# Kernel tuning notes

Measured on AMD Instinct MI355X. Metric: run time of the kernel, lower is better.

Reference implementation:

```python
import jax, jax.numpy as jnp
import numpy as np

B, N, D_IN, D_OUT, R = 8, 2048, 256, 256, 4


def setup_inputs() -> dict:
    key = jax.random.key(0)
    k1, k2, k3, k4 = jax.random.split(key, 4)
    x = jax.random.normal(k1, (B, N, D_IN), dtype=jnp.float32)
    adj = jnp.zeros((1,), dtype=jnp.float32)  # unused by the module
    # relation-type matrix: 0 = no edge, 1..R = relation id
    relation = jax.random.randint(k2, (B, N, N), 0, R + 1, dtype=jnp.int32)
    weight = jax.random.normal(k3, (R, D_IN, D_OUT), dtype=jnp.float32) * 0.05
    bias = jax.random.normal(k4, (D_OUT,), dtype=jnp.float32) * 0.05
    return {"x": x, "adj": adj, "relation": relation, "weight": weight, "bias": bias}


def reference(x, adj, relation, weight, bias):
    # Binary per-relation adjacency masks: [R, B, N, N]
    rel_ids = jnp.arange(1, weight.shape[0] + 1, dtype=relation.dtype)
    masks = (relation[None] == rel_ids[:, None, None, None]).astype(x.dtype)
    # Aggregate neighbors per relation: h[r] = A_r @ x  -> [R, B, N, D_in]
    h = jnp.einsum('rbnm,bmd->rbnd', masks, x)
    # Per-relation output transform, summed over relations: [B, N, D_out]
    y = jnp.einsum('rbnd,rdo->bno', h, weight)
    return y + bias
```

## Files before the change

kernel.cpp:

```cpp
#include <hip/hip_runtime.h>
#include <hip/hip_bf16.h>
#include <stdint.h>

typedef uint32_t u32;
typedef uint64_t u64;
typedef __bf16 bf16x8 __attribute__((ext_vector_type(8)));
typedef float f32x4 __attribute__((ext_vector_type(4)));
typedef u32 u32x4 __attribute__((ext_vector_type(4)));

#define NB 8
#define NN 2048
#define DIN 256
#define DOUT 256
#define NR 4
#define KTOT (NN * NR)

#define XW_BYTES   (NB * DOUT * KTOT * 2)
#define PART_BYTES (NB * NN * DOUT * 4)
#define WT_BYTES   (NR * DIN * DOUT * 2)
#define PART_ELEMS (NB * NN * DOUT)

__device__ __forceinline__ ushort f2bf(float f) {
  union { float f; u32 u; } c; c.f = f;
  return (ushort)((c.u + 0x7FFFu + ((c.u >> 16) & 1u)) >> 16);
}

__device__ __forceinline__ float bf2f(ushort u) {
  union { u32 i; float f; } c; c.i = ((u32)u) << 16; return c.f;
}

__device__ __forceinline__ void gload_lds16(const void* g, void* l) {
  __builtin_amdgcn_global_load_lds(
      (const __attribute__((address_space(1))) u32*)g,
      (__attribute__((address_space(3))) u32*)l, 16, 0, 0);
}

__global__ void k0_wT(const float* __restrict__ w, ushort* __restrict__ wT) {
  int i = blockIdx.x * 256 + threadIdx.x;
  int o = i & 255, d = (i >> 8) & 255, r = i >> 16;
  wT[(r * DOUT + o) * DIN + d] = f2bf(w[i]);
}

__global__ __launch_bounds__(512) void k1_xw(const float* __restrict__ x,
                                             const ushort* __restrict__ wT,
                                             ushort* __restrict__ xwT) {
  __shared__ char smem[65536];
  ushort* As = (ushort*)smem;
  ushort* Bs = (ushort*)(smem + 4096);
  const int t = threadIdx.x, l = t & 63, w = t >> 6;
  const int r = w >> 1, oh = w & 1;
  const int blk = blockIdx.x;
  const int b = blk >> 6, rest = blk & 63, mc = rest >> 1, ot = rest & 1;

  f32x4 acc[4][4] = {};
  const int arow = t >> 3, adc = (t & 7) << 2;
  const float* xg = x + ((size_t)(b * NN + mc * 64 + arow) * DIN + adc);

  for (int s = 0; s < 8; ++s) {
    const int d0 = s * 32;
    float4 xv = *(const float4*)(xg + d0);
    ushort4 a4;
    a4.x = f2bf(xv.x); a4.y = f2bf(xv.y); a4.z = f2bf(xv.z); a4.w = f2bf(xv.w);
    *(ushort4*)(As + arow * 32 + adc) = a4;
#pragma unroll
    for (int i = 0; i < 4; ++i) {
      int off = i * 4096 + t * 8;
      int rr = off >> 12, rem = off & 4095, o = rem >> 5, dd = rem & 31;
      const ushort* src = wT + ((size_t)(rr * DOUT + ot * 128 + o) * DIN + d0 + dd);
      gload_lds16(src, Bs + off);
    }
    __syncthreads();
    bf16x8 af[4];
#pragma unroll
    for (int fm = 0; fm < 4; ++fm)
      af[fm] = *(const bf16x8*)(As + (fm * 16 + (l & 15)) * 32 + (l >> 4) * 8);
#pragma unroll
    for (int fo = 0; fo < 4; ++fo) {
      bf16x8 bf = *(const bf16x8*)(Bs + (size_t)(r * 128 + oh * 64 + fo * 16 + (l & 15)) * 32 + (l >> 4) * 8);
#pragma unroll
      for (int fm = 0; fm < 4; ++fm)
        acc[fm][fo] = __builtin_amdgcn_mfma_f32_16x16x32_bf16(af[fm], bf, acc[fm][fo], 0, 0, 0);
    }
    __syncthreads();
  }
  ushort* Cs = (ushort*)smem;
#pragma unroll
  for (int fm = 0; fm < 4; ++fm)
#pragma unroll
    for (int fo = 0; fo < 4; ++fo)
#pragma unroll
      for (int j = 0; j < 4; ++j) {
        int o_loc = oh * 64 + fo * 16 + (l & 15);
        int ml = fm * 16 + (l >> 4) * 4 + j;
        Cs[o_loc * 256 + ml * 4 + r] = f2bf(acc[fm][fo][j]);
      }
  __syncthreads();
#pragma unroll
  for (int i = 0; i < 8; ++i) {
    int el = (i * 512 + t) * 8;
    int o_loc = el >> 8, kp = el & 255;
    *(uint4*)(xwT + (size_t)(b * DOUT + ot * 128 + o_loc) * KTOT + mc * 256 + kp) =
        *(const uint4*)(Cs + el);
  }
}

__global__ __launch_bounds__(512, 2) void k2_v2(const int* __restrict__ rel,
                                                const ushort* __restrict__ xwT,
                                                ushort* __restrict__ partb) {
  __shared__ char smem[131072];
  const int t = threadIdx.x, l = t & 63, w = t >> 6;
  const int wm = w >> 2, wn = w & 3;
  const int logical = (blockIdx.x & 7) * 32 + (blockIdx.x >> 3);
  const int b = logical >> 5;
  const int nt = (logical >> 2) & 7;
  const int ks = logical & 3;

  f32x4 acc[8][4] = {};
  const int fr = l & 15, fq = l >> 4;
  const int rswz = (fr & 7) << 4;

  char* const Ab0 = smem;
  char* const Ab1 = smem + 32768;
  char* const Bb0 = smem + 65536;
  char* const Bb1 = smem + 98304;

  const int arow = t >> 1, half = t & 1;
  const int aswz = (arow & 7) << 4;
  const int* relg = rel + ((size_t)(b * NN + nt * 256 + arow)) * NN + ks * 512 + half * 8;

  const int brow = t >> 3;
  const int kd = (((t & 7) ^ ((t >> 3) & 7)) << 3);
  const ushort* xwb = xwT + (size_t)b * DOUT * KTOT + ks * 2048;

  int4 rs0a, rs0b, rs1a, rs1b;

#define GLD_ALL(S, BB)                                                         \
  {                                                                            \
    _Pragma("unroll") for (int i = 0; i < 4; ++i)                              \
      gload_lds16(xwb + (size_t)(brow + 64 * i) * KTOT + (S) * 64 + kd,        \
                  (BB) + i * 8192 + t * 16);                                   \
  }

#define RELLOAD(S, RA, RB)                                                     \
  RA = *(const int4*)(relg + (S) * 16);                                        \
  RB = *(const int4*)(relg + (S) * 16 + 4);

#define EXPAND_A(ABASE, V0, V1)                                                \
  {                                                                            \
    char* rowp = (ABASE) + arow * 128;                                         \
    int vv[8] = {V0.x, V0.y, V0.z, V0.w, V1.x, V1.y, V1.z, V1.w};              \
    _Pragma("unroll") for (int p = 0; p < 4; ++p) {                            \
      int va = vv[2 * p], vb = vv[2 * p + 1];                                  \
      u32 sa = ((u32)(va - 1) & 3u) * 16u;                                     \
      u32 sb = ((u32)(vb - 1) & 3u) * 16u;                                     \
      u64 ha = va ? (0x3F80ull << sa) : 0ull;                                  \
      u64 hb = vb ? (0x3F80ull << sb) : 0ull;                                  \
      u32x4 e = {(u32)ha, (u32)(ha >> 32), (u32)hb, (u32)(hb >> 32)};          \
      *(u32x4*)(rowp + ((half * 64 + p * 16) ^ aswz)) = e;                     \
    }                                                                          \
  }

#define RDB(BV, BB, KK)                                                        \
  _Pragma("unroll") for (int fo = 0; fo < 4; ++fo)                             \
    BV[fo] = *(const bf16x8*)((BB) + (wn * 64 + fo * 16 + fr) * 128 +          \
                              (((KK) * 64 + fq * 16) ^ rswz));

#define RDA(AV, AB, FM0, KK)                                                   \
  _Pragma("unroll") for (int i = 0; i < 4; ++i)                                \
    AV[i] = *(const bf16x8*)((AB) + (wm * 128 + ((FM0) + i) * 16 + fr) * 128 + \
                             (((KK) * 64 + fq * 16) ^ rswz));

#define MFMA4(FM0, AV, BV)                                                     \
  __builtin_amdgcn_s_setprio(1);                                               \
  _Pragma("unroll") for (int i = 0; i < 4; ++i)                                \
    _Pragma("unroll") for (int fo = 0; fo < 4; ++fo)                           \
      acc[(FM0) + i][fo] = __builtin_amdgcn_mfma_f32_16x16x32_bf16(            \
          AV[i], BV[fo], acc[(FM0) + i][fo], 0, 0, 0);                         \
  __builtin_amdgcn_s_setprio(0);

#define ENDFENCE(VMS)                                                          \
  asm volatile("s_waitcnt vmcnt(" VMS ") lgkmcnt(0)" ::: "memory");            \
  __builtin_amdgcn_s_barrier();                                                \
  __builtin_amdgcn_sched_barrier(0);

#define STEP(S, P, Q, STG, REL, EXP, VMS)                                      \
  {                                                                            \
    bf16x8 b0[4], b1[4], aA[4], aB[4], aC[4], aD[4];                           \
    RDB(b0, Bb##P, 0);                                                         \
    RDA(aA, Ab##P, 0, 0);                                                      \
    if (STG) { GLD_ALL((S) + 1, Bb##Q); }                                      \
    __builtin_amdgcn_sched_barrier(0);                                         \
    if (REL) { RELLOAD((S) + 2, rs##P##a, rs##P##b); }                         \
    RDA(aB, Ab##P, 4, 0);                                                      \
    MFMA4(0, aA, b0);                                                          \
    RDA(aC, Ab##P, 0, 1);                                                      \
    if (EXP) { EXPAND_A(Ab##Q, rs##Q##a, rs##Q##b); }                          \
    MFMA4(4, aB, b0);                                                          \
    RDB(b1, Bb##P, 1);                                                         \
    RDA(aD, Ab##P, 4, 1);                                                      \
    MFMA4(0, aC, b1);                                                          \
    MFMA4(4, aD, b1);                                                          \
    ENDFENCE(VMS);                                                             \
  }

  GLD_ALL(0, Bb0);
  __builtin_amdgcn_sched_barrier(0);
  RELLOAD(0, rs0a, rs0b);
  RELLOAD(1, rs1a, rs1b);
  EXPAND_A(Ab0, rs0a, rs0b);
  ENDFENCE("4");

  for (int s = 0; s < 30; s += 2) {
    STEP(s, 0, 1, 1, 1, 1, "2");
    STEP(s + 1, 1, 0, 1, 1, 1, "2");
  }
  STEP(30, 0, 1, 1, 0, 1, "0");
  {
    bf16x8 b0[4], b1[4], aA[4], aB[4], aC[4], aD[4];
    RDB(b0, Bb1, 0);
    RDA(aA, Ab1, 0, 0);
    RDA(aB, Ab1, 4, 0);
    MFMA4(0, aA, b0);
    RDA(aC, Ab1, 0, 1);
    MFMA4(4, aB, b0);
    RDB(b1, Bb1, 1);
    RDA(aD, Ab1, 4, 1);
    MFMA4(0, aC, b1);
    MFMA4(4, aD, b1);
  }

  ushort* dst = partb + (size_t)ks * PART_ELEMS;
#pragma unroll
  for (int fm = 0; fm < 8; ++fm)
#pragma unroll
    for (int fo = 0; fo < 4; ++fo) {
      int n = nt * 256 + wm * 128 + fm * 16 + fq * 4;
      int o = wn * 64 + fo * 16 + fr;
#pragma unroll
      for (int j = 0; j < 4; ++j)
        dst[(size_t)(b * NN + n + j) * DOUT + o] = f2bf(acc[fm][fo][j]);
    }
#undef STEP
#undef ENDFENCE
#undef MFMA4
#undef RDA
#undef RDB
#undef EXPAND_A
#undef RELLOAD
#undef GLD_ALL
}

__global__ void k3_sum(float* __restrict__ out, const ushort* __restrict__ partb,
                       const float* __restrict__ bias) {
  int i = blockIdx.x * 256 + threadIdx.x;
  float4 s = ((const float4*)bias)[i & 63];
#pragma unroll
  for (int p = 0; p < 4; ++p) {
    ushort4 v = ((const ushort4*)(partb + (size_t)p * PART_ELEMS))[i];
    s.x += bf2f(v.x); s.y += bf2f(v.y); s.z += bf2f(v.z); s.w += bf2f(v.w);
  }
  ((float4*)out)[i] = s;
}

__global__ __launch_bounds__(256, 2) void k2_r4(const int* __restrict__ rel,
                                                const ushort* __restrict__ xwT,
                                                float* __restrict__ out,
                                                float* __restrict__ part) {
  __shared__ char smem[81920];
  const int t = threadIdx.x, l = t & 63, w = t >> 6;
  const int wr = w >> 1, wc = w & 1;
  const int logical = (blockIdx.x & 7) * 64 + (blockIdx.x >> 3);
  const int b = logical >> 6;
  const int nt = (logical >> 2) & 15;
  const int ks = (logical >> 1) & 1;
  const int ot = logical & 1;

  f32x4 acc[4][4] = {};
  const int arow = t >> 1, half = t & 1;
  const int* relg = rel + ((size_t)(b * NN + nt * 128 + arow) * NN + ks * 1024 + half * 8);
  const ushort* xwb = xwT + (size_t)(b * DOUT + ot * 128) * KTOT + ks * 4096;

  char* const Ab0 = smem;
  char* const Ab1 = smem + 16384;
  char* const Bb0 = smem + 32768;
  char* const Bb1 = smem + 49152;
  char* const Bb2 = smem + 65536;

  const int brow = t >> 3;
  const int kd = (((t & 7) ^ ((t >> 3) & 7)) << 3);
  const int aswz = (arow & 7) << 4;
  const int fr = l & 15, fq = l >> 4;
  const int rswz = (fr & 7) << 4;

  int4 rsA0, rsB0, rsA1, rsB1;

#define STAGE_B(S, BBASE)                                                      \
  {                                                                            \
    _Pragma("unroll") for (int i = 0; i < 4; ++i)                              \
      gload_lds16(xwb + (size_t)(brow + 32 * i) * KTOT + (S) * 64 + kd,        \
                  (BBASE) + i * 4096 + t * 16);                                \
  }
#define RELLOAD(S, RA, RB)                                                     \
  RA = *(const int4*)(relg + (S) * 16);                                        \
  RB = *(const int4*)(relg + (S) * 16 + 4);
#define EXPAND_A(ABASE, V0, V1)                                                \
  {                                                                            \
    char* rowp = (ABASE) + arow * 128;                                         \
    int vv[8] = {V0.x, V0.y, V0.z, V0.w, V1.x, V1.y, V1.z, V1.w};              \
    _Pragma("unroll") for (int p = 0; p < 4; ++p) {                            \
      int va = vv[2 * p], vb = vv[2 * p + 1];                                  \
      u32 sa = ((u32)(va - 1) & 3u) * 16u;                                     \
      u32 sb = ((u32)(vb - 1) & 3u) * 16u;                                     \
      u64 ha = va ? (0x3F80ull << sa) : 0ull;                                  \
      u64 hb = vb ? (0x3F80ull << sb) : 0ull;                                  \
      u32x4 e = {(u32)ha, (u32)(ha >> 32), (u32)hb, (u32)(hb >> 32)};          \
      *(u32x4*)(rowp + ((half * 64 + p * 16) ^ aswz)) = e;                     \
    }                                                                          \
  }
#define BARV6()                                                                \
  asm volatile("s_waitcnt vmcnt(6) lgkmcnt(0)" ::: "memory");                  \
  __builtin_amdgcn_s_barrier();                                                \
  __builtin_amdgcn_sched_barrier(0);
#define BARV0()                                                                \
  asm volatile("s_waitcnt vmcnt(0) lgkmcnt(0)" ::: "memory");                  \
  __builtin_amdgcn_s_barrier();                                                \
  __builtin_amdgcn_sched_barrier(0);
#define MFMA_STEP(AC, BC)                                                      \
  __builtin_amdgcn_s_setprio(1);                                               \
  _Pragma("unroll") for (int kk = 0; kk < 2; ++kk) {                           \
    bf16x8 af[4], bfv[4];                                                      \
    const int colb = (kk * 64 + fq * 16) ^ rswz;                               \
    _Pragma("unroll") for (int fm = 0; fm < 4; ++fm)                           \
      af[fm] = *(const bf16x8*)((AC) + (wr * 64 + fm * 16 + fr) * 128 + colb); \
    _Pragma("unroll") for (int fo = 0; fo < 4; ++fo)                           \
      bfv[fo] = *(const bf16x8*)((BC) + (wc * 64 + fo * 16 + fr) * 128 + colb);\
    _Pragma("unroll") for (int fm = 0; fm < 4; ++fm)                           \
      _Pragma("unroll") for (int fo = 0; fo < 4; ++fo)                         \
        acc[fm][fo] = __builtin_amdgcn_mfma_f32_16x16x32_bf16(                 \
            af[fm], bfv[fo], acc[fm][fo], 0, 0, 0);                            \
  }                                                                            \
  __builtin_amdgcn_s_setprio(0);
#define BODY(S, ACUR, BCUR, ANXT, RLA, RLB, RCA, RCB, BSTG)                    \
  {                                                                            \
    STAGE_B((S) + 2, BSTG);                                                    \
    RELLOAD((S) + 2, RLA, RLB);                                                \
    MFMA_STEP(ACUR, BCUR);                                                     \
    EXPAND_A(ANXT, RCA, RCB);                                                  \
    BARV6();                                                                   \
  }

  STAGE_B(0, Bb0);
  RELLOAD(0, rsA0, rsB0);
  STAGE_B(1, Bb1);
  RELLOAD(1, rsA1, rsB1);
  EXPAND_A(Ab0, rsA0, rsB0);
  BARV6();

  for (int s = 0; s < 60; s += 6) {
    BODY(s + 0, Ab0, Bb0, Ab1, rsA0, rsB0, rsA1, rsB1, Bb2);
    BODY(s + 1, Ab1, Bb1, Ab0, rsA1, rsB1, rsA0, rsB0, Bb0);
    BODY(s + 2, Ab0, Bb2, Ab1, rsA0, rsB0, rsA1, rsB1, Bb1);
    BODY(s + 3, Ab1, Bb0, Ab0, rsA1, rsB1, rsA0, rsB0, Bb2);
    BODY(s + 4, Ab0, Bb1, Ab1, rsA0, rsB0, rsA1, rsB1, Bb0);
    BODY(s + 5, Ab1, Bb2, Ab0, rsA1, rsB1, rsA0, rsB0, Bb1);
  }
  BODY(60, Ab0, Bb0, Ab1, rsA0, rsB0, rsA1, rsB1, Bb2);
  BODY(61, Ab1, Bb1, Ab0, rsA1, rsB1, rsA0, rsB0, Bb0);
  {
    MFMA_STEP(Ab0, Bb2);
    EXPAND_A(Ab1, rsA1, rsB1);
    BARV0();
  }
  {
    MFMA_STEP(Ab1, Bb0);
  }

  float* dst = ks ? part : out;
#pragma unroll
  for (int fm = 0; fm < 4; ++fm)
#pragma unroll
    for (int fo = 0; fo < 4; ++fo) {
      int n = nt * 128 + wr * 64 + fm * 16 + fq * 4;
      int o = ot * 128 + wc * 64 + fo * 16 + fr;
#pragma unroll
      for (int j = 0; j < 4; ++j)
        dst[(size_t)(b * NN + n + j) * DOUT + o] = acc[fm][fo][j];
    }
#undef BODY
#undef MFMA_STEP
#undef BARV6
#undef BARV0
#undef EXPAND_A
#undef RELLOAD
#undef STAGE_B
}

__global__ void k3_r4(float* __restrict__ out, const float* __restrict__ part,
                      const float* __restrict__ bias) {
  int i = blockIdx.x * 256 + threadIdx.x;
  float4 o = ((const float4*)out)[i];
  float4 p = ((const float4*)part)[i];
  float4 bv = ((const float4*)bias)[i & 63];
  float4 rr;
  rr.x = o.x + p.x + bv.x;
  rr.y = o.y + p.y + bv.y;
  rr.z = o.z + p.z + bv.z;
  rr.w = o.w + p.w + bv.w;
  ((float4*)out)[i] = rr;
}

extern "C" void kernel_launch(void* const* d_in, const int* in_sizes, int n_in,
                              void* d_out, int out_size, void* d_ws, size_t ws_size,
                              hipStream_t stream) {
  const float* x = (const float*)d_in[0];
  const int* rel = (const int*)d_in[2];
  const float* wgt = (const float*)d_in[3];
  const float* bias = (const float*)d_in[4];
  float* out = (float*)d_out;
  char* ws = (char*)d_ws;

  const size_t partb_bytes = (size_t)PART_ELEMS * 2 * 4;
  const size_t need_big = (size_t)XW_BYTES + partb_bytes + WT_BYTES;
  if (ws_size >= need_big) {
    ushort* xwT = (ushort*)ws;
    ushort* partb = (ushort*)(ws + XW_BYTES);
    ushort* wT = (ushort*)(ws + XW_BYTES + partb_bytes);
    k0_wT<<<1024, 256, 0, stream>>>(wgt, wT);
    k1_xw<<<512, 512, 0, stream>>>(x, wT, xwT);
    k2_v2<<<256, 512, 0, stream>>>(rel, xwT, partb);
    k3_sum<<<4096, 256, 0, stream>>>(out, partb, bias);
  } else {
    ushort* xwT = (ushort*)ws;
    float* part = (float*)(ws + XW_BYTES);
    ushort* wT = (ushort*)(ws + XW_BYTES + PART_BYTES);
    k0_wT<<<1024, 256, 0, stream>>>(wgt, wT);
    k1_xw<<<512, 512, 0, stream>>>(x, wT, xwT);
    k2_r4<<<512, 256, 0, stream>>>(rel, xwT, out, part);
    k3_r4<<<4096, 256, 0, stream>>>(out, part, bias);
  }
}
```

Measured before the change: 110.3 us.

## Stream raw relation ints into LDS via async loads and expand one-hot in registers

The main GEMM kernel used to load relation ids into registers, expand them into bf16 one-hot rows and write those to LDS each step. It now copies raw int32 relation tiles straight into LDS with global_load_lds, reads them back as int2 pairs, and builds the one-hot bf16x8 A fragments in registers right before each MFMA. This removes the LDS write and expansion phase from the critical path and puts both operands on the async DMA path, with A buffers covering two k-steps. In exchange it adds per-MFMA ALU work to build fragments, a new pipeline schedule with different vmcnt fences, and a dropped lgkmcnt wait.

```diff
diff --git a/kernel.cpp b/kernel.cpp
--- a/kernel.cpp
+++ b/kernel.cpp
@@ -33,6 +33,16 @@
   __builtin_amdgcn_global_load_lds(
       (const __attribute__((address_space(1))) u32*)g,
       (__attribute__((address_space(3))) u32*)l, 16, 0, 0);
+}
+
+__device__ __forceinline__ bf16x8 onehot8(int v0, int v1) {
+  u32 sa = ((u32)(v0 - 1) & 3u) * 16u;
+  u32 sb = ((u32)(v1 - 1) & 3u) * 16u;
+  u64 ha = v0 ? (0x3F80ull << sa) : 0ull;
+  u64 hb = v1 ? (0x3F80ull << sb) : 0ull;
+  union { u32x4 u; bf16x8 b; } c;
+  c.u = (u32x4){(u32)ha, (u32)(ha >> 32), (u32)hb, (u32)(hb >> 32)};
+  return c.b;
 }
 
 __global__ void k0_wT(const float* __restrict__ w, ushort* __restrict__ wT) {
@@ -104,7 +114,7 @@
   }
 }
 
-__global__ __launch_bounds__(512, 2) void k2_v2(const int* __restrict__ rel,
+__global__ __launch_bounds__(512, 2) void k2_v3(const int* __restrict__ rel,
                                                 const ushort* __restrict__ xwT,
                                                 ushort* __restrict__ partb) {
   __shared__ char smem[131072];
@@ -124,40 +134,26 @@
   char* const Bb0 = smem + 65536;
   char* const Bb1 = smem + 98304;
 
-  const int arow = t >> 1, half = t & 1;
-  const int aswz = (arow & 7) << 4;
-  const int* relg = rel + ((size_t)(b * NN + nt * 256 + arow)) * NN + ks * 512 + half * 8;
+  const int arow4 = t >> 3;
+  const int acol = ((t & 7) ^ ((t >> 3) & 7)) * 4;
+  const int* relg0 = rel + ((size_t)(b * NN + nt * 256)) * NN + ks * 512;
 
   const int brow = t >> 3;
   const int kd = (((t & 7) ^ ((t >> 3) & 7)) << 3);
   const ushort* xwb = xwT + (size_t)b * DOUT * KTOT + ks * 2048;
 
-  int4 rs0a, rs0b, rs1a, rs1b;
-
-#define GLD_ALL(S, BB)                                                         \
+#define GLD_B(S, BB)                                                           \
   {                                                                            \
     _Pragma("unroll") for (int i = 0; i < 4; ++i)                              \
       gload_lds16(xwb + (size_t)(brow + 64 * i) * KTOT + (S) * 64 + kd,        \
                   (BB) + i * 8192 + t * 16);                                   \
   }
 
-#define RELLOAD(S, RA, RB)                                                     \
-  RA = *(const int4*)(relg + (S) * 16);                                        \
-  RB = *(const int4*)(relg + (S) * 16 + 4);
-
-#define EXPAND_A(ABASE, V0, V1)                                                \
-  {                                                                            \
-    char* rowp = (ABASE) + arow * 128;                                         \
-    int vv[8] = {V0.x, V0.y, V0.z, V0.w, V1.x, V1.y, V1.z, V1.w};              \
-    _Pragma("unroll") for (int p = 0; p < 4; ++p) {                            \
-      int va = vv[2 * p], vb = vv[2 * p + 1];                                  \
-      u32 sa = ((u32)(va - 1) & 3u) * 16u;                                     \
-      u32 sb = ((u32)(vb - 1) & 3u) * 16u;                                     \
-      u64 ha = va ? (0x3F80ull << sa) : 0ull;                                  \
-      u64 hb = vb ? (0x3F80ull << sb) : 0ull;                                  \
-      u32x4 e = {(u32)ha, (u32)(ha >> 32), (u32)hb, (u32)(hb >> 32)};          \
-      *(u32x4*)(rowp + ((half * 64 + p * 16) ^ aswz)) = e;                     \
-    }                                                                          \
+#define GLD_A(P, AB)                                                           \
+  {                                                                            \
+    _Pragma("unroll") for (int i = 0; i < 4; ++i)                              \
+      gload_lds16(relg0 + (size_t)(arow4 + 64 * i) * NN + (P) * 32 + acol,     \
+                  (AB) + i * 8192 + t * 16);                                   \
   }
 
 #define RDB(BV, BB, KK)                                                        \
@@ -165,68 +161,71 @@
     BV[fo] = *(const bf16x8*)((BB) + (wn * 64 + fo * 16 + fr) * 128 +          \
                               (((KK) * 64 + fq * 16) ^ rswz));
 
-#define RDA(AV, AB, FM0, KK)                                                   \
-  _Pragma("unroll") for (int i = 0; i < 4; ++i)                                \
-    AV[i] = *(const bf16x8*)((AB) + (wm * 128 + ((FM0) + i) * 16 + fr) * 128 + \
-                             (((KK) * 64 + fq * 16) ^ rswz));
-
-#define MFMA4(FM0, AV, BV)                                                     \
+#define RDAREL(AR, AB, SIG)                                                    \
+  _Pragma("unroll") for (int f = 0; f < 8; ++f)                                \
+    _Pragma("unroll") for (int kq = 0; kq < 2; ++kq)                           \
+      AR[f * 2 + kq] = *(const int2*)((AB) + (wm * 128 + f * 16 + fr) * 128 +  \
+                                      (((SIG) * 64 + kq * 32 + fq * 8) ^ rswz));
+
+#define MFMAQ(FM0, AR, BV, KK)                                                 \
   __builtin_amdgcn_s_setprio(1);                                               \
-  _Pragma("unroll") for (int i = 0; i < 4; ++i)                                \
+  _Pragma("unroll") for (int i = 0; i < 4; ++i) {                              \
+    bf16x8 af = onehot8(AR[((FM0) + i) * 2 + (KK)].x,                          \
+                        AR[((FM0) + i) * 2 + (KK)].y);                         \
     _Pragma("unroll") for (int fo = 0; fo < 4; ++fo)                           \
       acc[(FM0) + i][fo] = __builtin_amdgcn_mfma_f32_16x16x32_bf16(            \
-          AV[i], BV[fo], acc[(FM0) + i][fo], 0, 0, 0);                         \
+          af, BV[fo], acc[(FM0) + i][fo], 0, 0, 0);                            \
+  }                                                                            \
   __builtin_amdgcn_s_setprio(0);
 
-#define ENDFENCE(VMS)                                                          \
-  asm volatile("s_waitcnt vmcnt(" VMS ") lgkmcnt(0)" ::: "memory");            \
+#define ENDF(VMS)                                                              \
+  asm volatile("s_waitcnt vmcnt(" VMS ")" ::: "memory");                       \
   __builtin_amdgcn_s_barrier();                                                \
   __builtin_amdgcn_sched_barrier(0);
 
-#define STEP(S, P, Q, STG, REL, EXP, VMS)                                      \
-  {                                                                            \
-    bf16x8 b0[4], b1[4], aA[4], aB[4], aC[4], aD[4];                           \
-    RDB(b0, Bb##P, 0);                                                         \
-    RDA(aA, Ab##P, 0, 0);                                                      \
-    if (STG) { GLD_ALL((S) + 1, Bb##Q); }                                      \
+#define STEP(S, PAIR, SIG, AB, BB, BN, AN, STGB, STGA, VMS)                    \
+  {                                                                            \
+    bf16x8 bv0[4], bv1[4];                                                     \
+    int2 ar[16];                                                               \
+    RDB(bv0, BB, 0);                                                           \
+    RDAREL(ar, AB, SIG);                                                       \
+    if (STGB) { GLD_B((S) + 1, BN); }                                          \
+    if (STGA) { GLD_A((PAIR) + 1, AN); }                                       \
     __builtin_amdgcn_sched_barrier(0);                                         \
-    if (REL) { RELLOAD((S) + 2, rs##P##a, rs##P##b); }                         \
-    RDA(aB, Ab##P, 4, 0);                                                      \
-    MFMA4(0, aA, b0);                                                          \
-    RDA(aC, Ab##P, 0, 1);                                                      \
-    if (EXP) { EXPAND_A(Ab##Q, rs##Q##a, rs##Q##b); }                          \
-    MFMA4(4, aB, b0);                                                          \
-    RDB(b1, Bb##P, 1);                                                         \
-    RDA(aD, Ab##P, 4, 1);                                                      \
-    MFMA4(0, aC, b1);                                                          \
-    MFMA4(4, aD, b1);                                                          \
-    ENDFENCE(VMS);                                                             \
-  }
-
-  GLD_ALL(0, Bb0);
+    MFMAQ(0, ar, bv0, 0);                                                      \
+    MFMAQ(4, ar, bv0, 0);                                                      \
+    RDB(bv1, BB, 1);                                                           \
+    MFMAQ(0, ar, bv1, 1);                                                      \
+    MFMAQ(4, ar, bv1, 1);                                                      \
+    ENDF(VMS);                                                                 \
+  }
+
+  GLD_A(0, Ab0);
+  GLD_B(0, Bb0);
+  asm volatile("s_waitcnt vmcnt(0)" ::: "memory");
+  __builtin_amdgcn_s_barrier();
   __builtin_amdgcn_sched_barrier(0);
-  RELLOAD(0, rs0a, rs0b);
-  RELLOAD(1, rs1a, rs1b);
-  EXPAND_A(Ab0, rs0a, rs0b);
-  ENDFENCE("4");
-
-  for (int s = 0; s < 30; s += 2) {
-    STEP(s, 0, 1, 1, 1, 1, "2");
-    STEP(s + 1, 1, 0, 1, 1, 1, "2");
-  }
-  STEP(30, 0, 1, 1, 0, 1, "0");
+
+  for (int i = 0; i < 7; ++i) {
+    const int s = i * 4, p = i * 2;
+    STEP(s + 0, p + 0, 0, Ab0, Bb0, Bb1, Ab1, 1, 1, "4");
+    STEP(s + 1, p + 0, 1, Ab0, Bb1, Bb0, Ab0, 1, 0, "0");
+    STEP(s + 2, p + 1, 0, Ab1, Bb0, Bb1, Ab0, 1, 1, "4");
+    STEP(s + 3, p + 1, 1, Ab1, Bb1, Bb0, Ab0, 1, 0, "0");
+  }
+  STEP(28, 14, 0, Ab0, Bb0, Bb1, Ab1, 1, 1, "4");
+  STEP(29, 14, 1, Ab0, Bb1, Bb0, Ab0, 1, 0, "0");
+  STEP(30, 15, 0, Ab1, Bb0, Bb1, Ab0, 1, 0, "0");
   {
-    bf16x8 b0[4], b1[4], aA[4], aB[4], aC[4], aD[4];
-    RDB(b0, Bb1, 0);
-    RDA(aA, Ab1, 0, 0);
-    RDA(aB, Ab1, 4, 0);
-    MFMA4(0, aA, b0);
-    RDA(aC, Ab1, 0, 1);
-    MFMA4(4, aB, b0);
-    RDB(b1, Bb1, 1);
-    RDA(aD, Ab1, 4, 1);
-    MFMA4(0, aC, b1);
-    MFMA4(4, aD, b1);
+    bf16x8 bv0[4], bv1[4];
+    int2 ar[16];
+    RDB(bv0, Bb1, 0);
+    RDAREL(ar, Ab1, 1);
+    MFMAQ(0, ar, bv0, 0);
+    MFMAQ(4, ar, bv0, 0);
+    RDB(bv1, Bb1, 1);
+    MFMAQ(0, ar, bv1, 1);
+    MFMAQ(4, ar, bv1, 1);
   }
 
   ushort* dst = partb + (size_t)ks * PART_ELEMS;
@@ -241,13 +240,12 @@
         dst[(size_t)(b * NN + n + j) * DOUT + o] = f2bf(acc[fm][fo][j]);
     }
 #undef STEP
-#undef ENDFENCE
-#undef MFMA4
-#undef RDA
+#undef ENDF
+#undef MFMAQ
+#undef RDAREL
 #undef RDB
-#undef EXPAND_A
-#undef RELLOAD
-#undef GLD_ALL
+#undef GLD_A
+#undef GLD_B
 }
 
 __global__ void k3_sum(float* __restrict__ out, const ushort* __restrict__ partb,
@@ -427,7 +425,7 @@
     ushort* wT = (ushort*)(ws + XW_BYTES + partb_bytes);
     k0_wT<<<1024, 256, 0, stream>>>(wgt, wT);
     k1_xw<<<512, 512, 0, stream>>>(x, wT, xwT);
-    k2_v2<<<256, 512, 0, stream>>>(rel, xwT, partb);
+    k2_v3<<<256, 512, 0, stream>>>(rel, xwT, partb);
     k3_sum<<<4096, 256, 0, stream>>>(out, partb, bias);
   } else {
     ushort* xwT = (ushort*)ws;
```

New measurement: 123.2 us. +11.7%, slower.

## Store relation A-tile as byte masks in LDS and expand to bf16 in registers

Applied to the files above, without the earlier changes.

The k2 main kernel now keeps the one-hot relation A operand in shared memory as 8-bit masks instead of expanded bf16 values. This halves the A-tile LDS footprint (shared memory drops from 128KB to 96KB) and halves the A-side LDS read and write traffic. Each MFMA A fragment is rebuilt in registers with v_perm and an AND against the bf16 1.0 pattern. The cost is extra VALU work per MFMA, and the reads and MFMAs are now grouped into whole half-steps, which changes how LDS reads overlap with compute.

```diff
diff --git a/kernel.cpp b/kernel.cpp
--- a/kernel.cpp
+++ b/kernel.cpp
@@ -33,6 +33,10 @@
   __builtin_amdgcn_global_load_lds(
       (const __attribute__((address_space(1))) u32*)g,
       (__attribute__((address_space(3))) u32*)l, 16, 0, 0);
+}
+
+__device__ __forceinline__ u32 relmask(int v) {
+  return v ? (0xFFu << (((u32)(v - 1) & 3u) * 8u)) : 0u;
 }
 
 __global__ void k0_wT(const float* __restrict__ w, ushort* __restrict__ wT) {
@@ -104,10 +108,10 @@
   }
 }
 
-__global__ __launch_bounds__(512, 2) void k2_v2(const int* __restrict__ rel,
+__global__ __launch_bounds__(512, 2) void k2_v5(const int* __restrict__ rel,
                                                 const ushort* __restrict__ xwT,
                                                 ushort* __restrict__ partb) {
-  __shared__ char smem[131072];
+  __shared__ char smem[98304];
   const int t = threadIdx.x, l = t & 63, w = t >> 6;
   const int wm = w >> 2, wn = w & 3;
   const int logical = (blockIdx.x & 7) * 32 + (blockIdx.x >> 3);
@@ -120,13 +124,14 @@
   const int rswz = (fr & 7) << 4;
 
   char* const Ab0 = smem;
-  char* const Ab1 = smem + 32768;
-  char* const Bb0 = smem + 65536;
-  char* const Bb1 = smem + 98304;
+  char* const Ab1 = smem + 16384;
+  char* const Bb0 = smem + 32768;
+  char* const Bb1 = smem + 65536;
 
   const int arow = t >> 1, half = t & 1;
-  const int aswz = (arow & 7) << 4;
   const int* relg = rel + ((size_t)(b * NN + nt * 256 + arow)) * NN + ks * 512 + half * 8;
+  char* const rowA0 = Ab0 + arow * 64;
+  char* const rowA1 = Ab1 + arow * 64;
 
   const int brow = t >> 3;
   const int kd = (((t & 7) ^ ((t >> 3) & 7)) << 3);
@@ -145,18 +150,12 @@
   RA = *(const int4*)(relg + (S) * 16);                                        \
   RB = *(const int4*)(relg + (S) * 16 + 4);
 
-#define EXPAND_A(ABASE, V0, V1)                                                \
-  {                                                                            \
-    char* rowp = (ABASE) + arow * 128;                                         \
+#define EXPAND_M(ROWP, V0, V1)                                                 \
+  {                                                                            \
     int vv[8] = {V0.x, V0.y, V0.z, V0.w, V1.x, V1.y, V1.z, V1.w};              \
-    _Pragma("unroll") for (int p = 0; p < 4; ++p) {                            \
-      int va = vv[2 * p], vb = vv[2 * p + 1];                                  \
-      u32 sa = ((u32)(va - 1) & 3u) * 16u;                                     \
-      u32 sb = ((u32)(vb - 1) & 3u) * 16u;                                     \
-      u64 ha = va ? (0x3F80ull << sa) : 0ull;                                  \
-      u64 hb = vb ? (0x3F80ull << sb) : 0ull;                                  \
-      u32x4 e = {(u32)ha, (u32)(ha >> 32), (u32)hb, (u32)(hb >> 32)};          \
-      *(u32x4*)(rowp + ((half * 64 + p * 16) ^ aswz)) = e;                     \
+    _Pragma("unroll") for (int jj = 0; jj < 4; ++jj) {                         \
+      u64 mw = (u64)relmask(vv[2 * jj]) | ((u64)relmask(vv[2 * jj + 1]) << 32);\
+      *(u64*)((ROWP) + (((half * 4 + jj) ^ (arow & 7)) * 8)) = mw;             \
     }                                                                          \
   }
 
@@ -165,50 +164,58 @@
     BV[fo] = *(const bf16x8*)((BB) + (wn * 64 + fo * 16 + fr) * 128 +          \
                               (((KK) * 64 + fq * 16) ^ rswz));
 
-#define RDA(AV, AB, FM0, KK)                                                   \
-  _Pragma("unroll") for (int i = 0; i < 4; ++i)                                \
-    AV[i] = *(const bf16x8*)((AB) + (wm * 128 + ((FM0) + i) * 16 + fr) * 128 + \
-                             (((KK) * 64 + fq * 16) ^ rswz));
-
-#define MFMA4(FM0, AV, BV)                                                     \
+#define RDA_K(AR, AB, KK)                                                      \
+  _Pragma("unroll") for (int f = 0; f < 8; ++f)                                \
+    AR[f] = *(const int2*)((AB) + (wm * 128 + f * 16 + fr) * 64 +              \
+                           ((((KK) * 4 + fq) ^ (fr & 7)) * 8));
+
+#define MFMA1(FM, Q, BV)                                                       \
+  {                                                                            \
+    u32x4 uu;                                                                  \
+    uu.x = __builtin_amdgcn_perm((u32)(Q).x, (u32)(Q).x, 0x01010000u) & 0x3F803F80u; \
+    uu.y = __builtin_amdgcn_perm((u32)(Q).x, (u32)(Q).x, 0x03030202u) & 0x3F803F80u; \
+    uu.z = __builtin_amdgcn_perm((u32)(Q).y, (u32)(Q).y, 0x01010000u) & 0x3F803F80u; \
+    uu.w = __builtin_amdgcn_perm((u32)(Q).y, (u32)(Q).y, 0x03030202u) & 0x3F803F80u; \
+    union { u32x4 u; bf16x8 b; } cv; cv.u = uu;                                \
+    _Pragma("unroll") for (int fo = 0; fo < 4; ++fo)                           \
+      acc[FM][fo] = __builtin_amdgcn_mfma_f32_16x16x32_bf16(                   \
+          cv.b, BV[fo], acc[FM][fo], 0, 0, 0);                                 \
+  }
+
+#define MFMAH(AR, BV)                                                          \
   __builtin_amdgcn_s_setprio(1);                                               \
-  _Pragma("unroll") for (int i = 0; i < 4; ++i)                                \
-    _Pragma("unroll") for (int fo = 0; fo < 4; ++fo)                           \
-      acc[(FM0) + i][fo] = __builtin_amdgcn_mfma_f32_16x16x32_bf16(            \
-          AV[i], BV[fo], acc[(FM0) + i][fo], 0, 0, 0);                         \
+  _Pragma("unroll") for (int f = 0; f < 8; ++f) MFMA1(f, AR[f], BV);           \
   __builtin_amdgcn_s_setprio(0);
 
-#define ENDFENCE(VMS)                                                          \
+#define ENDF(VMS)                                                              \
   asm volatile("s_waitcnt vmcnt(" VMS ") lgkmcnt(0)" ::: "memory");            \
   __builtin_amdgcn_s_barrier();                                                \
   __builtin_amdgcn_sched_barrier(0);
 
 #define STEP(S, P, Q, STG, REL, EXP, VMS)                                      \
   {                                                                            \
-    bf16x8 b0[4], b1[4], aA[4], aB[4], aC[4], aD[4];                           \
-    RDB(b0, Bb##P, 0);                                                         \
-    RDA(aA, Ab##P, 0, 0);                                                      \
+    bf16x8 bv0[4], bv1[4];                                                     \
+    int2 a0[8], a1[8];                                                         \
+    RDB(bv0, Bb##P, 0);                                                        \
+    RDA_K(a0, Ab##P, 0);                                                       \
     if (STG) { GLD_ALL((S) + 1, Bb##Q); }                                      \
     __builtin_amdgcn_sched_barrier(0);                                         \
     if (REL) { RELLOAD((S) + 2, rs##P##a, rs##P##b); }                         \
-    RDA(aB, Ab##P, 4, 0);                                                      \
-    MFMA4(0, aA, b0);                                                          \
-    RDA(aC, Ab##P, 0, 1);                                                      \
-    if (EXP) { EXPAND_A(Ab##Q, rs##Q##a, rs##Q##b); }                          \
-    MFMA4(4, aB, b0);                                                          \
-    RDB(b1, Bb##P, 1);                                                         \
-    RDA(aD, Ab##P, 4, 1);                                                      \
-    MFMA4(0, aC, b1);                                                          \
-    MFMA4(4, aD, b1);                                                          \
-    ENDFENCE(VMS);                                                             \
+    __builtin_amdgcn_sched_barrier(0);                                         \
+    MFMAH(a0, bv0);                                                            \
+    RDB(bv1, Bb##P, 1);                                                        \
+    RDA_K(a1, Ab##P, 1);                                                       \
+    if (EXP) { EXPAND_M(rowA##Q, rs##Q##a, rs##Q##b); }                        \
+    MFMAH(a1, bv1);                                                            \
+    ENDF(VMS);                                                                 \
   }
 
   GLD_ALL(0, Bb0);
   __builtin_amdgcn_sched_barrier(0);
   RELLOAD(0, rs0a, rs0b);
   RELLOAD(1, rs1a, rs1b);
-  EXPAND_A(Ab0, rs0a, rs0b);
-  ENDFENCE("4");
+  EXPAND_M(rowA0, rs0a, rs0b);
+  ENDF("4");
 
   for (int s = 0; s < 30; s += 2) {
     STEP(s, 0, 1, 1, 1, 1, "2");
@@ -216,17 +223,14 @@
   }
   STEP(30, 0, 1, 1, 0, 1, "0");
   {
-    bf16x8 b0[4], b1[4], aA[4], aB[4], aC[4], aD[4];
-    RDB(b0, Bb1, 0);
-    RDA(aA, Ab1, 0, 0);
-    RDA(aB, Ab1, 4, 0);
-    MFMA4(0, aA, b0);
-    RDA(aC, Ab1, 0, 1);
-    MFMA4(4, aB, b0);
-    RDB(b1, Bb1, 1);
-    RDA(aD, Ab1, 4, 1);
-    MFMA4(0, aC, b1);
-    MFMA4(4, aD, b1);
+    bf16x8 bv0[4], bv1[4];
+    int2 a0[8], a1[8];
+    RDB(bv0, Bb1, 0);
+    RDA_K(a0, Ab1, 0);
+    MFMAH(a0, bv0);
+    RDB(bv1, Bb1, 1);
+    RDA_K(a1, Ab1, 1);
+    MFMAH(a1, bv1);
   }
 
   ushort* dst = partb + (size_t)ks * PART_ELEMS;
@@ -241,11 +245,12 @@
         dst[(size_t)(b * NN + n + j) * DOUT + o] = f2bf(acc[fm][fo][j]);
     }
 #undef STEP
-#undef ENDFENCE
-#undef MFMA4
-#undef RDA
+#undef ENDF
+#undef MFMAH
+#undef MFMA1
+#undef RDA_K
 #undef RDB
-#undef EXPAND_A
+#undef EXPAND_M
 #undef RELLOAD
 #undef GLD_ALL
 }
@@ -427,7 +432,7 @@
     ushort* wT = (ushort*)(ws + XW_BYTES + partb_bytes);
     k0_wT<<<1024, 256, 0, stream>>>(wgt, wT);
     k1_xw<<<512, 512, 0, stream>>>(x, wT, xwT);
-    k2_v2<<<256, 512, 0, stream>>>(rel, xwT, partb);
+    k2_v5<<<256, 512, 0, stream>>>(rel, xwT, partb);
     k3_sum<<<4096, 256, 0, stream>>>(out, partb, bias);
   } else {
     ushort* xwT = (ushort*)ws;
```

Result: slower. 115.1 us (+4.3%).

## Double-buffer and swizzle LDS tiles in the x·W precompute kernel

Applied to the files above, without the earlier changes.

Rewrites the k1_xw main loop to double-buffer the A and B tiles in LDS, prefetching the next K-slice of weights and x while MFMAs run on the current one, with one barrier per step instead of two. It also applies an XOR swizzle to the LDS layouts to reduce bank conflicts on fragment reads, and raises wave priority around the MFMA block. LDS use grows from 64 KB to 72 KB, which can reduce occupancy, and k1 is probably a small share of total time next to k2.

```diff
diff --git a/kernel.cpp b/kernel.cpp
--- a/kernel.cpp
+++ b/kernel.cpp
@@ -44,45 +44,93 @@
 __global__ __launch_bounds__(512) void k1_xw(const float* __restrict__ x,
                                              const ushort* __restrict__ wT,
                                              ushort* __restrict__ xwT) {
-  __shared__ char smem[65536];
-  ushort* As = (ushort*)smem;
-  ushort* Bs = (ushort*)(smem + 4096);
+  __shared__ char smem[73728];
+  char* const Ab0 = smem;
+  char* const Ab1 = smem + 4096;
+  char* const Bb0 = smem + 8192;
+  char* const Bb1 = smem + 40960;
   const int t = threadIdx.x, l = t & 63, w = t >> 6;
   const int r = w >> 1, oh = w & 1;
   const int blk = blockIdx.x;
   const int b = blk >> 6, rest = blk & 63, mc = rest >> 1, ot = rest & 1;
 
   f32x4 acc[4][4] = {};
-  const int arow = t >> 3, adc = (t & 7) << 2;
-  const float* xg = x + ((size_t)(b * NN + mc * 64 + arow) * DIN + adc);
-
-  for (int s = 0; s < 8; ++s) {
-    const int d0 = s * 32;
-    float4 xv = *(const float4*)(xg + d0);
-    ushort4 a4;
-    a4.x = f2bf(xv.x); a4.y = f2bf(xv.y); a4.z = f2bf(xv.z); a4.w = f2bf(xv.w);
-    *(ushort4*)(As + arow * 32 + adc) = a4;
-#pragma unroll
-    for (int i = 0; i < 4; ++i) {
-      int off = i * 4096 + t * 8;
-      int rr = off >> 12, rem = off & 4095, o = rem >> 5, dd = rem & 31;
-      const ushort* src = wT + ((size_t)(rr * DOUT + ot * 128 + o) * DIN + d0 + dd);
-      gload_lds16(src, Bs + off);
-    }
-    __syncthreads();
-    bf16x8 af[4];
-#pragma unroll
-    for (int fm = 0; fm < 4; ++fm)
-      af[fm] = *(const bf16x8*)(As + (fm * 16 + (l & 15)) * 32 + (l >> 4) * 8);
-#pragma unroll
-    for (int fo = 0; fo < 4; ++fo) {
-      bf16x8 bf = *(const bf16x8*)(Bs + (size_t)(r * 128 + oh * 64 + fo * 16 + (l & 15)) * 32 + (l >> 4) * 8);
-#pragma unroll
-      for (int fm = 0; fm < 4; ++fm)
-        acc[fm][fo] = __builtin_amdgcn_mfma_f32_16x16x32_bf16(af[fm], bf, acc[fm][fo], 0, 0, 0);
-    }
-    __syncthreads();
-  }
+  const int fr = l & 15, fq = l >> 4;
+  const int ru = ((fq ^ (fr & 3)) << 4);
+
+  const int arow = t >> 3;
+  const int abyte = ((((t & 7) >> 1) ^ (arow & 3)) << 4) + (t & 1) * 8;
+  const float* xg = x + ((size_t)(b * NN + mc * 64 + arow) * DIN + (t & 7) * 4);
+
+  const int bdd = (((t & 3) ^ ((t >> 2) & 3)) << 3);
+  const int bro = (t >> 2);
+
+#define K1_GLDB(D0, BB)                                                        \
+  {                                                                            \
+    _Pragma("unroll") for (int i = 0; i < 4; ++i) {                            \
+      const ushort* src = wT + ((size_t)(i * DOUT + ot * 128 + bro) * DIN +    \
+                                (D0) + bdd);                                   \
+      gload_lds16(src, (BB) + i * 8192 + t * 16);                              \
+    }                                                                          \
+  }
+
+#define K1_WRA(AB, XV)                                                         \
+  {                                                                            \
+    ushort4 a4;                                                                \
+    a4.x = f2bf((XV).x); a4.y = f2bf((XV).y);                                  \
+    a4.z = f2bf((XV).z); a4.w = f2bf((XV).w);                                  \
+    *(ushort4*)((AB) + arow * 64 + abyte) = a4;                                \
+  }
+
+#define K1_MFMA(AB, BB)                                                        \
+  {                                                                            \
+    bf16x8 af[4];                                                              \
+    __builtin_amdgcn_s_setprio(1);                                             \
+    _Pragma("unroll") for (int fm = 0; fm < 4; ++fm)                           \
+      af[fm] = *(const bf16x8*)((AB) + (fm * 16 + fr) * 64 + ru);              \
+    _Pragma("unroll") for (int fo = 0; fo < 4; ++fo) {                         \
+      bf16x8 bf = *(const bf16x8*)((BB) + (size_t)(r * 128 + oh * 64 +         \
+                                   fo * 16 + fr) * 64 + ru);                   \
+      _Pragma("unroll") for (int fm = 0; fm < 4; ++fm)                         \
+        acc[fm][fo] = __builtin_amdgcn_mfma_f32_16x16x32_bf16(                 \
+            af[fm], bf, acc[fm][fo], 0, 0, 0);                                 \
+    }                                                                          \
+    __builtin_amdgcn_s_setprio(0);                                             \
+  }
+
+#define K1_ENDF()                                                              \
+  asm volatile("s_waitcnt vmcnt(0) lgkmcnt(0)" ::: "memory");                  \
+  __builtin_amdgcn_s_barrier();                                                \
+  __builtin_amdgcn_sched_barrier(0);
+
+#define K1_STEP(S, AP, BP, AQ, BQ)                                             \
+  {                                                                            \
+    K1_GLDB((S + 1) * 32, BQ);                                                 \
+    __builtin_amdgcn_sched_barrier(0);                                         \
+    float4 xv = *(const float4*)(xg + (S + 1) * 32);                           \
+    K1_MFMA(AP, BP);                                                           \
+    K1_WRA(AQ, xv);                                                            \
+    K1_ENDF();                                                                 \
+  }
+
+  K1_GLDB(0, Bb0);
+  __builtin_amdgcn_sched_barrier(0);
+  {
+    float4 xv = *(const float4*)(xg);
+    K1_WRA(Ab0, xv);
+  }
+  K1_ENDF();
+
+  K1_STEP(0, Ab0, Bb0, Ab1, Bb1);
+  K1_STEP(1, Ab1, Bb1, Ab0, Bb0);
+  K1_STEP(2, Ab0, Bb0, Ab1, Bb1);
+  K1_STEP(3, Ab1, Bb1, Ab0, Bb0);
+  K1_STEP(4, Ab0, Bb0, Ab1, Bb1);
+  K1_STEP(5, Ab1, Bb1, Ab0, Bb0);
+  K1_STEP(6, Ab0, Bb0, Ab1, Bb1);
+  K1_MFMA(Ab1, Bb1);
+  __syncthreads();
+
   ushort* Cs = (ushort*)smem;
 #pragma unroll
   for (int fm = 0; fm < 4; ++fm)
@@ -90,8 +138,8 @@
     for (int fo = 0; fo < 4; ++fo)
 #pragma unroll
       for (int j = 0; j < 4; ++j) {
-        int o_loc = oh * 64 + fo * 16 + (l & 15);
-        int ml = fm * 16 + (l >> 4) * 4 + j;
+        int o_loc = oh * 64 + fo * 16 + fr;
+        int ml = fm * 16 + fq * 4 + j;
         Cs[o_loc * 256 + ml * 4 + r] = f2bf(acc[fm][fo][j]);
       }
   __syncthreads();
@@ -102,6 +150,11 @@
     *(uint4*)(xwT + (size_t)(b * DOUT + ot * 128 + o_loc) * KTOT + mc * 256 + kp) =
         *(const uint4*)(Cs + el);
   }
+#undef K1_STEP
+#undef K1_ENDF
+#undef K1_MFMA
+#undef K1_WRA
+#undef K1_GLDB
 }
 
 __global__ __launch_bounds__(512, 2) void k2_v2(const int* __restrict__ rel,
```

After: 108.4 us (median of 2 runs). No clear change (-1.7%).
